# Kernel tuning notes

Measured on AMD Instinct MI355X. Metric: run time of the kernel, lower is better.

Reference implementation:

```python
import jax, jax.numpy as jnp
import numpy as np

S, E, K, D = 20000, 10000, 128, 128   # students, exercises, knowledge, latent dim
N_EK, N_SE = 40000, 500000            # exercise-knowledge edges, student-exercise edges
B = 2048                              # extract batch size


def setup_inputs() -> dict:
    key = jax.random.key(0)
    ks = jax.random.split(key, 16)
    inp = {}
    # Embedding tables (xavier-ish scale)
    inp["stu_emb"] = jax.random.normal(ks[0], (S, D), jnp.float32) * 0.1
    inp["exer_emb"] = jax.random.normal(ks[1], (E, D), jnp.float32) * 0.1
    inp["kn_emb"] = jax.random.normal(ks[2], (K, D), jnp.float32) * 0.1
    inp["disc_emb"] = jax.random.normal(ks[3], (E, 1), jnp.float32) * 0.1
    # GraphLayer params, stacked over [fusion_layer=2, graph={k_from_e,e_from_k,s_from_e,e_from_s}]
    inp["GW"] = jax.random.normal(ks[4], (2, 4, D, D), jnp.float32) * (1.0 / np.sqrt(D))
    inp["Ga"] = jax.random.normal(ks[5], (2, 4, 2 * D), jnp.float32) * 0.1
    # Fusion attention fcs: idx 0=e_attn_fc1, 1=e_attn_fc2, 2=k_attn_fc3 (weight [2D], bias scalar)
    inp["Fw"] = jax.random.normal(ks[6], (2, 3, 2 * D), jnp.float32) * 0.1
    inp["Fb"] = jax.random.normal(ks[7], (2, 3), jnp.float32) * 0.1
    # q_mask (unused by extract, part of the signature)
    inp["q_mask"] = jax.random.bernoulli(ks[8], 0.03, (B, K)).astype(jnp.float32)
    inp["student_id"] = jax.random.randint(ks[9], (B,), 0, S, jnp.int32)
    inp["exercise_id"] = jax.random.randint(ks[10], (B,), 0, E, jnp.int32)
    # k_from_e graph: nodes = [exercises 0..E) ++ [knowledge E..E+K); edges exercise -> knowledge
    inp["ek_src"] = jax.random.randint(ks[11], (N_EK,), 0, E, jnp.int32)
    inp["ek_dst"] = E + jax.random.randint(ks[12], (N_EK,), 0, K, jnp.int32)
    # s_from_e graph: nodes = [exercises 0..E) ++ [students E..E+S); edges exercise -> student
    inp["se_src"] = jax.random.randint(ks[13], (N_SE,), 0, E, jnp.int32)
    inp["se_dst"] = E + jax.random.randint(ks[14], (N_SE,), 0, S, jnp.int32)
    return inp


def _graph_layer(h, W, a, src, dst, n):
    # GAT-style: z = h W; per-edge score a^T [z_src; z_dst]; segment softmax over dst; weighted sum of z_src.
    z = h @ W                                   # [n, D]
    zs, zd = z[src], z[dst]                     # [ne, D] gathers
    e = jnp.concatenate([zs, zd], axis=1) @ a   # [ne]
    emax = jax.ops.segment_max(e, dst, num_segments=n)
    emax = jnp.where(jnp.isfinite(emax), emax, 0.0)  # empty segments -> -inf -> 0
    ex = jnp.exp(e - emax[dst])
    den = jax.ops.segment_sum(ex, dst, num_segments=n)
    alpha = ex / jnp.where(den > 0, den, 1.0)[dst]
    return jax.ops.segment_sum(alpha[:, None] * zs, dst, num_segments=n)  # nodes w/o mail -> 0 (DGL semantics)


def _fusion(kn, ex, st, GWl, Gal, Fwl, Fbl, ek_src, ek_dst, se_src, se_dst):
    nek, nes = E + K, E + S
    ekg = jnp.concatenate([ex, kn], axis=0)
    kfe = _graph_layer(ekg, GWl[0], Gal[0], ek_src, ek_dst, nek)  # k_from_e
    efk = _graph_layer(ekg, GWl[1], Gal[1], ek_dst, ek_src, nek)  # e_from_k (reversed edges)
    esg = jnp.concatenate([ex, st], axis=0)
    ufe = _graph_layer(esg, GWl[2], Gal[2], se_src, se_dst, nes)  # s_from_e
    efu = _graph_layer(esg, GWl[3], Gal[3], se_dst, se_src, nes)  # e_from_s (reversed edges)
    # knowledge update: softmax over a single column == 1 (faithful to original)
    Dk = kfe[E:]
    s3 = jax.nn.softmax((jnp.concatenate([kn, Dk], axis=1) @ Fwl[2] + Fbl[2])[:, None], axis=1)
    kn2 = kn + s3[:, 0:1] * Dk
    # exercise update: 2-way softmax gate
    Bx, Cx = efk[:E], efu[:E]
    s1 = jnp.concatenate([ex, Bx], axis=1) @ Fwl[0] + Fbl[0]
    s2 = jnp.concatenate([ex, Cx], axis=1) @ Fwl[1] + Fbl[1]
    sc = jax.nn.softmax(jnp.stack([s1, s2], axis=1), axis=1)  # [E, 2]
    ex2 = ex + sc[:, 0:1] * Bx + sc[:, 1:2] * Cx
    st2 = st + ufe[E:]
    return kn2, ex2, st2


def reference(stu_emb, exer_emb, kn_emb, disc_emb, GW, Ga, Fw, Fb, q_mask,
              student_id, exercise_id, ek_src, ek_dst, se_src, se_dst):
    kn, ex, st = kn_emb, exer_emb, stu_emb
    for l in range(2):  # FusionLayer1, FusionLayer2
        kn, ex, st = _fusion(kn, ex, st, GW[l], Ga[l], Fw[l], Fb[l],
                             ek_src, ek_dst, se_src, se_dst)
    bs = st[student_id]            # [B, D]
    be = ex[exercise_id]           # [B, D]
    disc = disc_emb[exercise_id]   # [B, 1]
    # if_type == 'rcd': repeat(1,D).reshape(B,D,D) == broadcast along axis 1
    stu_ts = jnp.broadcast_to(bs[:, None, :], (B, D, D))
    exer_ts = jnp.broadcast_to(be[:, None, :], (B, D, D))
    kn_ts = jnp.broadcast_to(kn[None, :, :], (B, K, D))
    return (stu_ts, exer_ts, disc, kn_ts)
```

## Files before the change

kernel.cpp:

```cpp
#include <hip/hip_runtime.h>

#define S_N 20000
#define E_N 10000
#define K_N 128
#define D_N 128
#define NEK 40000
#define NSE 500000
#define B_N 2048

typedef __attribute__((ext_vector_type(8))) short bf16x8;
typedef __attribute__((ext_vector_type(4))) float f32x4;

__device__ __forceinline__ unsigned short f2bf(float f){
  unsigned int u = __float_as_uint(f);
  unsigned int r = u + 0x7FFFu + ((u >> 16) & 1u);
  return (unsigned short)(r >> 16);
}
__device__ __forceinline__ float bf2f(unsigned short h){
  return __uint_as_float(((unsigned int)h) << 16);
}

struct GS { const unsigned short* Ah; const unsigned short* Al;
            const unsigned short* Wh; const unsigned short* Wl;
            unsigned short* Z; int rows; };
struct CSet { const int* cnt; int n; int* rp; int* cur; };

#define HB ((NSE+255)/256)
__global__ __launch_bounds__(256) void k_hist(const int* __restrict__ eks, const int* __restrict__ ekd,
      const int* __restrict__ ses, const int* __restrict__ sed,
      int* c_eke, int* c_ekk, int* c_see, int* c_ses,
      const float* __restrict__ GW, const float* __restrict__ Ga,
      unsigned short* __restrict__ wf, float* __restrict__ wa){
  int bb = blockIdx.x;
  if(bb >= HB){
    int g = bb - HB;
    const float* W  = GW + (size_t)g*16384;
    const float* a1 = Ga + (size_t)g*256;
    unsigned short* whi = wf + (size_t)g*16384;
    unsigned short* wlo = wf + (size_t)(8+g)*16384;
    int t = threadIdx.x, l = t & 63;
    for(int pi = t>>6; pi < 32; pi += 4){
      int c2 = pi >> 2, kt = pi & 3;
      unsigned short h[8], lo[8];
      #pragma unroll
      for(int j=0;j<8;j++){
        int k = kt*32 + (l>>4)*8 + j;
        int c = c2*16 + (l&15);
        float f = W[(size_t)k*128 + c];
        unsigned short hb = f2bf(f);
        h[j] = hb; lo[j] = f2bf(f - bf2f(hb));
      }
      size_t off = ((size_t)pi*64 + l)*8;
      uint4 hv, lv;
      hv.x = (unsigned)h[0] | ((unsigned)h[1]<<16);  hv.y = (unsigned)h[2] | ((unsigned)h[3]<<16);
      hv.z = (unsigned)h[4] | ((unsigned)h[5]<<16);  hv.w = (unsigned)h[6] | ((unsigned)h[7]<<16);
      lv.x = (unsigned)lo[0] | ((unsigned)lo[1]<<16); lv.y = (unsigned)lo[2] | ((unsigned)lo[3]<<16);
      lv.z = (unsigned)lo[4] | ((unsigned)lo[5]<<16); lv.w = (unsigned)lo[6] | ((unsigned)lo[7]<<16);
      *(uint4*)(whi + off) = hv;
      *(uint4*)(wlo + off) = lv;
    }
    for(int k = t; k < 128; k += 256){
      float s = 0.f;
      const float* wr = W + (size_t)k*128;
      for(int c=0;c<128;c++) s += wr[c]*a1[c];
      wa[(size_t)g*128 + k] = s;
    }
    return;
  }
  int i = bb*256 + threadIdx.x;
  if(i < NEK){ atomicAdd(c_eke + eks[i], 1); atomicAdd(c_ekk + (ekd[i]-E_N), 1); }
  if(i < NSE){ atomicAdd(c_see + ses[i], 1); atomicAdd(c_ses + (sed[i]-E_N), 1); }
}

__global__ __launch_bounds__(1024) void k_scan(CSet c0, CSet c1, CSet c2, CSet c3){
  CSet c = c0;
  if(blockIdx.x==1) c=c1; else if(blockIdx.x==2) c=c2; else if(blockIdx.x==3) c=c3;
  __shared__ int part[1024];
  int t = threadIdx.x;
  int n = c.n;
  int chunk = (n + 1023) >> 10;
  int b0 = t * chunk;
  int s = 0;
  for(int i=0;i<chunk;i++){ int idx=b0+i; if(idx<n) s += c.cnt[idx]; }
  part[t] = s;
  __syncthreads();
  for(int off=1; off<1024; off<<=1){
    int v = (t>=off) ? part[t-off] : 0;
    __syncthreads();
    part[t] += v;
    __syncthreads();
  }
  int run = t ? part[t-1] : 0;
  for(int i=0;i<chunk;i++){
    int idx=b0+i;
    if(idx<n){ int cc = c.cnt[idx]; c.rp[idx]=run; c.cur[idx]=run; run += cc; }
  }
  if(t==0) c.rp[n] = part[1023];
}

__global__ __launch_bounds__(256) void k_fill(const int* __restrict__ eks, const int* __restrict__ ekd,
      const int* __restrict__ ses, const int* __restrict__ sed,
      int* u_eke, int* u_ekk, int* u_see, int* u_ses,
      int* o_eke, int* o_ekk, int* o_see, int* o_ses){
  int i = blockIdx.x*256 + threadIdx.x;
  if(i < NEK){
    int a = eks[i], b = ekd[i];
    int pos = atomicAdd(u_eke + a, 1);        o_eke[pos] = b;
    int pos2 = atomicAdd(u_ekk + (b-E_N), 1); o_ekk[pos2] = a;
  }
  if(i < NSE){
    int a = ses[i], b = sed[i];
    int pos = atomicAdd(u_see + a, 1);        o_see[pos] = b;
    int pos2 = atomicAdd(u_ses + (b-E_N), 1); o_ses[pos2] = a;
  }
}

__global__ __launch_bounds__(256) void k_cvt(const float* __restrict__ kn, const float* __restrict__ ex,
    const float* __restrict__ st,
    unsigned short* __restrict__ knb, unsigned short* __restrict__ exb, unsigned short* __restrict__ stb,
    const float* __restrict__ wa, int l4,
    float* __restrict__ Pefk, float* __restrict__ Pkfe, float* __restrict__ Pufe, float* __restrict__ Pefu){
  int w = (blockIdx.x*256 + threadIdx.x) >> 6;
  int lane = threadIdx.x & 63;
  const float* src; unsigned short *hi, *lo; int r;
  const float* wv1; const float* wv2 = nullptr; float *P1, *P2 = nullptr;
  if(w < K_N){ r = w; src = kn + (size_t)r*128; hi = knb; lo = knb + (size_t)K_N*128;
               wv1 = wa + (size_t)(l4+1)*128; P1 = Pefk; }
  else if(w < K_N + E_N){ r = w - K_N; src = ex + (size_t)r*128; hi = exb; lo = exb + (size_t)E_N*128;
               wv1 = wa + (size_t)(l4+0)*128; P1 = Pkfe;
               wv2 = wa + (size_t)(l4+2)*128; P2 = Pufe; }
  else { r = w - K_N - E_N; if(r >= S_N) return; src = st + (size_t)r*128; hi = stb; lo = stb + (size_t)S_N*128;
               wv1 = wa + (size_t)(l4+3)*128; P1 = Pefu; }
  float2 x = ((const float2*)src)[lane];
  float2 v1 = ((const float2*)wv1)[lane];
  float d1 = x.x*v1.x + x.y*v1.y;
  float d2 = 0.f;
  if(wv2){ float2 v2 = ((const float2*)wv2)[lane]; d2 = x.x*v2.x + x.y*v2.y; }
  #pragma unroll
  for(int off=1; off<64; off<<=1){ d1 += __shfl_xor(d1,off); d2 += __shfl_xor(d2,off); }
  if(lane==0){ P1[r] = expf(d1); if(P2) P2[r] = expf(d2); }
  unsigned short h0 = f2bf(x.x), h1 = f2bf(x.y);
  unsigned short l0 = f2bf(x.x - bf2f(h0)), l1 = f2bf(x.y - bf2f(h1));
  ((ushort2*)(hi + (size_t)r*128))[lane] = make_ushort2(h0,h1);
  ((ushort2*)(lo + (size_t)r*128))[lane] = make_ushort2(l0,l1);
}

#define GT0 4
#define GT1 317
#define GT2 942
#define GT3 1255
__global__ __launch_bounds__(256) void k_gemm(GS g0, GS g1, GS g2, GS g3){
  int b = blockIdx.x;
  GS g; int lt;
  if(b < GT0){ g = g0; lt = b; }
  else if(b < GT1){ g = g1; lt = b - GT0; }
  else if(b < GT2){ g = g2; lt = b - GT1; }
  else { g = g3; lt = b - GT2; }
  int l = threadIdx.x & 63, wv = threadIdx.x >> 6;
  int r0 = lt*32;
  bf16x8 bh[2][4], bl[2][4];
  #pragma unroll
  for(int cs=0; cs<2; cs++)
    #pragma unroll
    for(int kt=0; kt<4; kt++){
      size_t o = (((size_t)((wv*2+cs)*4 + kt))*64 + l)*8;
      bh[cs][kt] = *(const bf16x8*)(g.Wh + o);
      bl[cs][kt] = *(const bf16x8*)(g.Wl + o);
    }
  f32x4 acc[2][2];
  #pragma unroll
  for(int rs=0;rs<2;rs++)
    #pragma unroll
    for(int cs=0;cs<2;cs++) acc[rs][cs] = (f32x4){0.f,0.f,0.f,0.f};
  #pragma unroll
  for(int kt=0; kt<4; kt++){
    bf16x8 ah[2], al[2];
    #pragma unroll
    for(int rs=0; rs<2; rs++){
      size_t ao = ((size_t)(r0 + rs*16 + (l&15)))*128 + kt*32 + (l>>4)*8;
      ah[rs] = *(const bf16x8*)(g.Ah + ao);
      al[rs] = *(const bf16x8*)(g.Al + ao);
    }
    #pragma unroll
    for(int rs=0; rs<2; rs++)
      #pragma unroll
      for(int cs=0; cs<2; cs++){
        acc[rs][cs] = __builtin_amdgcn_mfma_f32_16x16x32_bf16(ah[rs], bh[cs][kt], acc[rs][cs], 0,0,0);
        acc[rs][cs] = __builtin_amdgcn_mfma_f32_16x16x32_bf16(ah[rs], bl[cs][kt], acc[rs][cs], 0,0,0);
        acc[rs][cs] = __builtin_amdgcn_mfma_f32_16x16x32_bf16(al[rs], bh[cs][kt], acc[rs][cs], 0,0,0);
      }
  }
  #pragma unroll
  for(int rs=0; rs<2; rs++)
    #pragma unroll
    for(int cs=0; cs<2; cs++){
      int cb = (wv<<5) + (cs<<4) + (l&15);
      #pragma unroll
      for(int j=0;j<4;j++){
        float v = acc[rs][cs][j];
        float vp = __shfl_xor(v, 1);
        int rr = r0 + rs*16 + ((l>>4)<<2) + j;
        if(!(l&1) && rr < g.rows){
          unsigned int pw = (unsigned)f2bf(v) | ((unsigned)f2bf(vp)<<16);
          *(unsigned int*)(g.Z + (size_t)rr*128 + cb) = pw;
        }
      }
    }
}

#define BFACC(zz, xx) \
  a[0] += xx*__uint_as_float(zz.x<<16); a[1] += xx*__uint_as_float(zz.x&0xffff0000u); \
  a[2] += xx*__uint_as_float(zz.y<<16); a[3] += xx*__uint_as_float(zz.y&0xffff0000u); \
  a[4] += xx*__uint_as_float(zz.z<<16); a[5] += xx*__uint_as_float(zz.z&0xffff0000u); \
  a[6] += xx*__uint_as_float(zz.w<<16); a[7] += xx*__uint_as_float(zz.w&0xffff0000u);

__device__ __forceinline__ void seg_row_q(const unsigned short* __restrict__ z, const float* __restrict__ p,
                                          const int* __restrict__ col, int e0, int e1,
                                          int q, int l16, float* a, float& denO){
  #pragma unroll
  for(int j=0;j<8;j++) a[j] = 0.f;
  float den = 0.f;
  const unsigned short* zl = z + l16*8;
  int e = e0 + q;
  for(; e + 12 < e1; e += 16){
    int cA = col[e], cB = col[e+4], cC = col[e+8], cD = col[e+12];
    float xA = p[cA], xB = p[cB], xC = p[cC], xD = p[cD];
    uint4 zA = *(const uint4*)(zl + (size_t)cA*128);
    uint4 zB = *(const uint4*)(zl + (size_t)cB*128);
    uint4 zC = *(const uint4*)(zl + (size_t)cC*128);
    uint4 zD = *(const uint4*)(zl + (size_t)cD*128);
    BFACC(zA,xA) BFACC(zB,xB) BFACC(zC,xC) BFACC(zD,xD)
    den += (xA + xB) + (xC + xD);
  }
  for(; e < e1; e += 4){
    int cA = col[e];
    float xA = p[cA];
    uint4 zA = *(const uint4*)(zl + (size_t)cA*128);
    BFACC(zA,xA)
    den += xA;
  }
  #pragma unroll
  for(int j=0;j<8;j++){ a[j] += __shfl_xor(a[j],16); a[j] += __shfl_xor(a[j],32); }
  den += __shfl_xor(den,16); den += __shfl_xor(den,32);
  denO = den;
}

#define S2A 2500
#define S2B 7500
#define S2C 7628
__global__ __launch_bounds__(256) void k_seg2(
    const unsigned short* __restrict__ zB, const float* __restrict__ pB, const int* __restrict__ rpB, const int* __restrict__ colB,
    const unsigned short* __restrict__ zC, const float* __restrict__ pC, const int* __restrict__ rpC, const int* __restrict__ colC,
    const unsigned short* __restrict__ zS, const float* __restrict__ pS, const int* __restrict__ rpS, const int* __restrict__ colS,
    const float* __restrict__ stBase, float* __restrict__ stOut,
    const unsigned short* __restrict__ zK, const float* __restrict__ pK, const int* __restrict__ rpK, const int* __restrict__ colK,
    const float* __restrict__ knBase, float* __restrict__ knOut,
    const float* __restrict__ exBase, float* __restrict__ exOut,
    const float* __restrict__ Fwl, const float* __restrict__ Fbl){
  __shared__ float4 red0[4][16];
  __shared__ float4 red1[4][16];
  __shared__ float redd[4];
  int b = blockIdx.x;
  int lane = threadIdx.x & 63, wid = threadIdx.x >> 6;
  int q = lane >> 4, l16 = lane & 15;
  if(b < S2A){
    int row = b*4 + wid;
    float B[8], C[8]; float dB, dC;
    seg_row_q(zB, pB, colB, rpB[row], rpB[row+1], q, l16, B, dB);
    seg_row_q(zC, pC, colC, rpC[row], rpC[row+1], q, l16, C, dC);
    float invB = dB > 0.f ? 1.f/dB : 0.f;
    float invC = dC > 0.f ? 1.f/dC : 0.f;
    #pragma unroll
    for(int j=0;j<8;j++){ B[j]*=invB; C[j]*=invC; }
    const float4* exr = (const float4*)(exBase + (size_t)row*128) + l16*2;
    float4 ea = exr[0], eb = exr[1];
    float ex8[8] = {ea.x,ea.y,ea.z,ea.w, eb.x,eb.y,eb.z,eb.w};
    float s1 = 0.f, s2 = 0.f;
    #pragma unroll
    for(int j=0;j<8;j++){
      s1 += ex8[j]*Fwl[l16*8+j]       + B[j]*Fwl[128+l16*8+j];
      s2 += ex8[j]*Fwl[256+l16*8+j]   + C[j]*Fwl[384+l16*8+j];
    }
    #pragma unroll
    for(int off=1; off<16; off<<=1){ s1 += __shfl_xor(s1,off); s2 += __shfl_xor(s2,off); }
    s1 += Fbl[0]; s2 += Fbl[1];
    float mx = fmaxf(s1,s2);
    float pp = expf(s1-mx), qq = expf(s2-mx);
    float iv = 1.f/(pp+qq);
    pp *= iv; qq *= iv;
    if(q==0){
      float o8[8];
      #pragma unroll
      for(int j=0;j<8;j++) o8[j] = ex8[j] + pp*B[j] + qq*C[j];
      float4* orow = (float4*)(exOut + (size_t)row*128) + l16*2;
      orow[0] = (float4){o8[0],o8[1],o8[2],o8[3]};
      orow[1] = (float4){o8[4],o8[5],o8[6],o8[7]};
    }
  } else if(b < S2B){
    int row = (b-S2A)*4 + wid;
    float a[8]; float den;
    seg_row_q(zS, pS, colS, rpS[row], rpS[row+1], q, l16, a, den);
    float inv = den > 0.f ? 1.f/den : 0.f;
    if(q==0){
      const float4* br = (const float4*)(stBase + (size_t)row*128) + l16*2;
      float4 b0 = br[0], b1 = br[1];
      float4* orow = (float4*)(stOut + (size_t)row*128) + l16*2;
      orow[0] = (float4){a[0]*inv + b0.x, a[1]*inv + b0.y, a[2]*inv + b0.z, a[3]*inv + b0.w};
      orow[1] = (float4){a[4]*inv + b1.x, a[5]*inv + b1.y, a[6]*inv + b1.z, a[7]*inv + b1.w};
    }
  } else {
    int row = b - S2B;
    int e0 = rpK[row], e1 = rpK[row+1];
    float a[8];
    #pragma unroll
    for(int j=0;j<8;j++) a[j]=0.f;
    float den = 0.f;
    const unsigned short* zl = zK + l16*8;
    int str = wid*4 + q;
    int e = e0 + str;
    for(; e + 48 < e1; e += 64){
      int cA = colK[e], cB = colK[e+16], cC = colK[e+32], cD = colK[e+48];
      float xA = pK[cA], xB = pK[cB], xC = pK[cC], xD = pK[cD];
      uint4 zA = *(const uint4*)(zl + (size_t)cA*128);
      uint4 zB = *(const uint4*)(zl + (size_t)cB*128);
      uint4 zC = *(const uint4*)(zl + (size_t)cC*128);
      uint4 zD = *(const uint4*)(zl + (size_t)cD*128);
      BFACC(zA,xA) BFACC(zB,xB) BFACC(zC,xC) BFACC(zD,xD)
      den += (xA + xB) + (xC + xD);
    }
    for(; e < e1; e += 16){
      int cA = colK[e];
      float xA = pK[cA];
      uint4 zA = *(const uint4*)(zl + (size_t)cA*128);
      BFACC(zA,xA)
      den += xA;
    }
    #pragma unroll
    for(int j=0;j<8;j++){ a[j] += __shfl_xor(a[j],16); a[j] += __shfl_xor(a[j],32); }
    den += __shfl_xor(den,16); den += __shfl_xor(den,32);
    if(lane < 16){
      red0[wid][l16] = (float4){a[0],a[1],a[2],a[3]};
      red1[wid][l16] = (float4){a[4],a[5],a[6],a[7]};
      if(l16==0) redd[wid] = den;
    }
    __syncthreads();
    if(wid) return;
    float4 a0 = red0[0][l16], a1 = red1[0][l16]; den = redd[0];
    #pragma unroll
    for(int i=1;i<4;i++){
      float4 r0 = red0[i][l16], r1 = red1[i][l16];
      a0.x+=r0.x; a0.y+=r0.y; a0.z+=r0.z; a0.w+=r0.w;
      a1.x+=r1.x; a1.y+=r1.y; a1.z+=r1.z; a1.w+=r1.w;
      den += redd[i];
    }
    float inv = den > 0.f ? 1.f/den : 0.f;
    if(q==0){
      const float4* br = (const float4*)(knBase + (size_t)row*128) + l16*2;
      float4 b0 = br[0], b1 = br[1];
      float4* orow = (float4*)(knOut + (size_t)row*128) + l16*2;
      orow[0] = (float4){a0.x*inv + b0.x, a0.y*inv + b0.y, a0.z*inv + b0.z, a0.w*inv + b0.w};
      orow[1] = (float4){a1.x*inv + b1.x, a1.y*inv + b1.y, a1.z*inv + b1.z, a1.w*inv + b1.w};
    }
  }
}

__global__ __launch_bounds__(256) void k_out(const float* __restrict__ st, const float* __restrict__ ex,
    const float* __restrict__ kn, const float* __restrict__ disc,
    const int* __restrict__ sid, const int* __restrict__ eid,
    float* out0, float* out1, float* out2, float* out3){
  int w = (blockIdx.x*256 + threadIdx.x) >> 6;
  int lane = threadIdx.x & 63;
  const int ROWW = 3*B_N*64;
  if(w < ROWW){
    int half = lane>>5, l32 = lane&31;
    int r = w*2 + half;
    int sec = r >> 18;
    int rr = r & 262143;
    int b = rr >> 7, i = rr & 127;
    const float* emb; int srow; float* ob;
    if(sec==0){ emb=st; srow=sid[b]; ob=out0; }
    else if(sec==1){ emb=ex; srow=eid[b]; ob=out1; }
    else { emb=kn; srow=i; ob=out3; }
    f32x4 v = *((const f32x4*)(emb + (size_t)srow*128) + l32);
    __builtin_nontemporal_store(v, (f32x4*)(ob + (size_t)rr*128) + l32);
  } else {
    int i = (w - ROWW)*64 + lane;
    if(i < B_N) out2[i] = disc[eid[i]];
  }
}

extern "C" void kernel_launch(void* const* d_in, const int* in_sizes, int n_in,
                              void* d_out, int out_size, void* d_ws, size_t ws_size,
                              hipStream_t stream){
  (void)in_sizes; (void)out_size; (void)ws_size;
  const float* stu_emb  = (const float*)d_in[0];
  const float* exer_emb = (const float*)d_in[1];
  const float* kn_emb   = (const float*)d_in[2];
  const float* disc_emb = (const float*)d_in[3];
  const float* GW = (const float*)d_in[4];
  const float* Ga = (const float*)d_in[5];
  const float* Fw = (const float*)d_in[6];
  const float* Fb = (const float*)d_in[7];
  int base = n_in - 6;
  const int* sid    = (const int*)d_in[base];
  const int* eid    = (const int*)d_in[base+1];
  const int* ek_src = (const int*)d_in[base+2];
  const int* ek_dst = (const int*)d_in[base+3];
  const int* se_src = (const int*)d_in[base+4];
  const int* se_dst = (const int*)d_in[base+5];

  char* w = (char*)d_ws;
  size_t off = 0;
  auto alloc = [&](size_t bytes)->char*{ char* p = w + off; off += (bytes + 255) & ~(size_t)255; return p; };
  float* st_f = (float*)alloc((size_t)S_N*D_N*4);
  float* ex_f = (float*)alloc((size_t)E_N*D_N*4);
  float* kn_f = (float*)alloc((size_t)K_N*D_N*4);
  unsigned short* zefk = (unsigned short*)alloc((size_t)K_N*D_N*2);
  unsigned short* zkfe = (unsigned short*)alloc((size_t)E_N*D_N*2);
  unsigned short* zefu = (unsigned short*)alloc((size_t)S_N*D_N*2);
  unsigned short* zufe = (unsigned short*)alloc((size_t)E_N*D_N*2);
  float* Pefk = (float*)alloc((size_t)K_N*4);
  float* Pkfe = (float*)alloc((size_t)E_N*4);
  float* Pefu = (float*)alloc((size_t)S_N*4);
  float* Pufe = (float*)alloc((size_t)E_N*4);
  unsigned short* knb = (unsigned short*)alloc((size_t)K_N*D_N*2*2 + 4096);
  unsigned short* exb = (unsigned short*)alloc((size_t)E_N*D_N*2*2 + 4096);
  unsigned short* stb = (unsigned short*)alloc((size_t)S_N*D_N*2*2 + 4096);
  unsigned short* wf  = (unsigned short*)alloc((size_t)16*16384*2);
  float* wa   = (float*)alloc((size_t)8*128*4);
  int*   cnt  = (int*)alloc((size_t)(2*E_N+K_N+S_N)*4);
  int*   rp   = (int*)alloc((size_t)(2*(E_N+1)+(K_N+1)+(S_N+1))*4);
  int*   cur  = (int*)alloc((size_t)(2*E_N+K_N+S_N)*4);
  int*   col  = (int*)alloc((size_t)(2*NEK+2*NSE)*4);

  int* cnt_eke = cnt;                 int* cnt_ekk = cnt + E_N;
  int* cnt_see = cnt + E_N + K_N;     int* cnt_ses = cnt + 2*E_N + K_N;
  int* cur_eke = cur;                 int* cur_ekk = cur + E_N;
  int* cur_see = cur + E_N + K_N;     int* cur_ses = cur + 2*E_N + K_N;
  int* rp_eke = rp;                                int* rp_ekk = rp + (E_N+1);
  int* rp_see = rp + (E_N+1) + (K_N+1);            int* rp_ses = rp + 2*(E_N+1) + (K_N+1);
  int* col_eke = col;                 int* col_ekk = col + NEK;
  int* col_see = col + 2*NEK;         int* col_ses = col + 2*NEK + NSE;

  hipMemsetAsync(cnt, 0, (size_t)(2*E_N+K_N+S_N)*4, stream);
  k_hist<<<HB+8,256,0,stream>>>(ek_src, ek_dst, se_src, se_dst,
                                cnt_eke, cnt_ekk, cnt_see, cnt_ses,
                                GW, Ga, wf, wa);
  k_scan<<<4,1024,0,stream>>>(CSet{cnt_eke,E_N,rp_eke,cur_eke}, CSet{cnt_ekk,K_N,rp_ekk,cur_ekk},
                              CSet{cnt_see,E_N,rp_see,cur_see}, CSet{cnt_ses,S_N,rp_ses,cur_ses});
  k_fill<<<HB,256,0,stream>>>(ek_src, ek_dst, se_src, se_dst,
                              cur_eke, cur_ekk, cur_see, cur_ses,
                              col_eke, col_ekk, col_see, col_ses);

  const unsigned short* knb_lo = knb + (size_t)K_N*128;
  const unsigned short* exb_lo = exb + (size_t)E_N*128;
  const unsigned short* stb_lo = stb + (size_t)S_N*128;

  for(int l=0; l<2; l++){
    const float* knp = l ? kn_f : kn_emb;
    const float* exp_ = l ? ex_f : exer_emb;
    const float* stp = l ? st_f : stu_emb;
    int l4 = l*4;
    k_cvt<<<(K_N+E_N+S_N)/4,256,0,stream>>>(knp, exp_, stp, knb, exb, stb, wa, l4,
                                            Pefk, Pkfe, Pufe, Pefu);
    GS g0{knb, knb_lo, wf + (size_t)(l4+1)*16384, wf + (size_t)(8+l4+1)*16384, zefk, K_N};
    GS g1{exb, exb_lo, wf + (size_t)(l4+0)*16384, wf + (size_t)(8+l4+0)*16384, zkfe, E_N};
    GS g2{stb, stb_lo, wf + (size_t)(l4+3)*16384, wf + (size_t)(8+l4+3)*16384, zefu, S_N};
    GS g3{exb, exb_lo, wf + (size_t)(l4+2)*16384, wf + (size_t)(8+l4+2)*16384, zufe, E_N};
    k_gemm<<<GT3,256,0,stream>>>(g0,g1,g2,g3);
    k_seg2<<<S2C,256,0,stream>>>(
      zefk - (size_t)E_N*128, Pefk - E_N, rp_eke, col_eke,
      zefu - (size_t)E_N*128, Pefu - E_N, rp_see, col_see,
      zufe, Pufe, rp_ses, col_ses, stp, st_f,
      zkfe, Pkfe, rp_ekk, col_ekk, knp, kn_f,
      exp_, ex_f, Fw + (size_t)l*3*2*D_N, Fb + (size_t)l*3);
  }

  float* out  = (float*)d_out;
  float* out0 = out;
  float* out1 = out0 + (size_t)B_N*D_N*D_N;
  float* out2 = out1 + (size_t)B_N*D_N*D_N;
  float* out3 = out2 + (size_t)B_N;
  int waves = 3*B_N*64 + 32;
  k_out<<<(waves+3)/4,256,0,stream>>>(st_f, ex_f, kn_f, disc_emb, sid, eid, out0, out1, out2, out3);
}
```

Before: 746.0 us.

## Map one row per 16-lane quarter-wave in segment aggregation kernel

```diff
diff --git a/kernel.cpp b/kernel.cpp
--- a/kernel.cpp
+++ b/kernel.cpp
@@ -214,16 +214,16 @@
   a[4] += xx*__uint_as_float(zz.z<<16); a[5] += xx*__uint_as_float(zz.z&0xffff0000u); \
   a[6] += xx*__uint_as_float(zz.w<<16); a[7] += xx*__uint_as_float(zz.w&0xffff0000u);
 
-__device__ __forceinline__ void seg_row_q(const unsigned short* __restrict__ z, const float* __restrict__ p,
-                                          const int* __restrict__ col, int e0, int e1,
-                                          int q, int l16, float* a, float& denO){
+__device__ __forceinline__ void seg_row_q4(const unsigned short* __restrict__ z, const float* __restrict__ p,
+                                           const int* __restrict__ col, int e0, int e1,
+                                           int l16, float* a, float& denO){
   #pragma unroll
   for(int j=0;j<8;j++) a[j] = 0.f;
   float den = 0.f;
   const unsigned short* zl = z + l16*8;
-  int e = e0 + q;
-  for(; e + 12 < e1; e += 16){
-    int cA = col[e], cB = col[e+4], cC = col[e+8], cD = col[e+12];
+  int e = e0;
+  for(; e + 3 < e1; e += 4){
+    int cA = col[e], cB = col[e+1], cC = col[e+2], cD = col[e+3];
     float xA = p[cA], xB = p[cB], xC = p[cC], xD = p[cD];
     uint4 zA = *(const uint4*)(zl + (size_t)cA*128);
     uint4 zB = *(const uint4*)(zl + (size_t)cB*128);
@@ -232,22 +232,19 @@
     BFACC(zA,xA) BFACC(zB,xB) BFACC(zC,xC) BFACC(zD,xD)
     den += (xA + xB) + (xC + xD);
   }
-  for(; e < e1; e += 4){
+  for(; e < e1; e++){
     int cA = col[e];
     float xA = p[cA];
     uint4 zA = *(const uint4*)(zl + (size_t)cA*128);
     BFACC(zA,xA)
     den += xA;
   }
-  #pragma unroll
-  for(int j=0;j<8;j++){ a[j] += __shfl_xor(a[j],16); a[j] += __shfl_xor(a[j],32); }
-  den += __shfl_xor(den,16); den += __shfl_xor(den,32);
   denO = den;
 }
 
-#define S2A 2500
-#define S2B 7500
-#define S2C 7628
+#define S2A 625
+#define S2B 1875
+#define S2C 2003
 __global__ __launch_bounds__(256) void k_seg2(
     const unsigned short* __restrict__ zB, const float* __restrict__ pB, const int* __restrict__ rpB, const int* __restrict__ colB,
     const unsigned short* __restrict__ zC, const float* __restrict__ pC, const int* __restrict__ rpC, const int* __restrict__ colC,
@@ -264,10 +261,10 @@
   int lane = threadIdx.x & 63, wid = threadIdx.x >> 6;
   int q = lane >> 4, l16 = lane & 15;
   if(b < S2A){
-    int row = b*4 + wid;
+    int row = b*16 + wid*4 + q;
     float B[8], C[8]; float dB, dC;
-    seg_row_q(zB, pB, colB, rpB[row], rpB[row+1], q, l16, B, dB);
-    seg_row_q(zC, pC, colC, rpC[row], rpC[row+1], q, l16, C, dC);
+    seg_row_q4(zB, pB, colB, rpB[row], rpB[row+1], l16, B, dB);
+    seg_row_q4(zC, pC, colC, rpC[row], rpC[row+1], l16, C, dC);
     float invB = dB > 0.f ? 1.f/dB : 0.f;
     float invC = dC > 0.f ? 1.f/dC : 0.f;
     #pragma unroll
@@ -288,26 +285,21 @@
     float pp = expf(s1-mx), qq = expf(s2-mx);
     float iv = 1.f/(pp+qq);
     pp *= iv; qq *= iv;
-    if(q==0){
-      float o8[8];
-      #pragma unroll
-      for(int j=0;j<8;j++) o8[j] = ex8[j] + pp*B[j] + qq*C[j];
-      float4* orow = (float4*)(exOut + (size_t)row*128) + l16*2;
-      orow[0] = (float4){o8[0],o8[1],o8[2],o8[3]};
-      orow[1] = (float4){o8[4],o8[5],o8[6],o8[7]};
-    }
+    float4* orow = (float4*)(exOut + (size_t)row*128) + l16*2;
+    orow[0] = (float4){ex8[0] + pp*B[0] + qq*C[0], ex8[1] + pp*B[1] + qq*C[1],
+                       ex8[2] + pp*B[2] + qq*C[2], ex8[3] + pp*B[3] + qq*C[3]};
+    orow[1] = (float4){ex8[4] + pp*B[4] + qq*C[4], ex8[5] + pp*B[5] + qq*C[5],
+                       ex8[6] + pp*B[6] + qq*C[6], ex8[7] + pp*B[7] + qq*C[7]};
   } else if(b < S2B){
-    int row = (b-S2A)*4 + wid;
+    int row = (b-S2A)*16 + wid*4 + q;
     float a[8]; float den;
-    seg_row_q(zS, pS, colS, rpS[row], rpS[row+1], q, l16, a, den);
+    seg_row_q4(zS, pS, colS, rpS[row], rpS[row+1], l16, a, den);
     float inv = den > 0.f ? 1.f/den : 0.f;
-    if(q==0){
-      const float4* br = (const float4*)(stBase + (size_t)row*128) + l16*2;
-      float4 b0 = br[0], b1 = br[1];
-      float4* orow = (float4*)(stOut + (size_t)row*128) + l16*2;
-      orow[0] = (float4){a[0]*inv + b0.x, a[1]*inv + b0.y, a[2]*inv + b0.z, a[3]*inv + b0.w};
-      orow[1] = (float4){a[4]*inv + b1.x, a[5]*inv + b1.y, a[6]*inv + b1.z, a[7]*inv + b1.w};
-    }
+    const float4* br = (const float4*)(stBase + (size_t)row*128) + l16*2;
+    float4 b0 = br[0], b1 = br[1];
+    float4* orow = (float4*)(stOut + (size_t)row*128) + l16*2;
+    orow[0] = (float4){a[0]*inv + b0.x, a[1]*inv + b0.y, a[2]*inv + b0.z, a[3]*inv + b0.w};
+    orow[1] = (float4){a[4]*inv + b1.x, a[5]*inv + b1.y, a[6]*inv + b1.z, a[7]*inv + b1.w};
   } else {
     int row = b - S2B;
     int e0 = rpK[row], e1 = rpK[row+1];
```

Measured after the change: 730.9 us. -2.0%, faster.
